# Kernel optimization log

Hardware: AMD Instinct MI355X
Metric: run time of the kernel (lower is better)

Reference implementation:

```python
import jax, jax.numpy as jnp
import numpy as np

N_NODES = 400      # total nodes across batch
B = 10             # graphs in batch (40 nodes each)
N_CONFIGS = 1000   # fixed by tile dataset
CONFIG_FEAT_DIM = 24
NODE_FEAT_DIM = 85  # continuous cols; node_feat has +1 col for shape-ele-type idx
N_SHAPE_TYPES = 8
SHAPE_EMB = 4
N_OPS = 120
OP_EMB = 32
H = 64             # h_dim
E = 800            # edges
CAT_DIM = NODE_FEAT_DIM + SHAPE_EMB + OP_EMB + CONFIG_FEAT_DIM  # 145


def _lin(k, i, o):
    return jax.random.normal(k, (i, o), jnp.float32) * (1.0 / np.sqrt(i))


def setup_inputs() -> dict:
    key = jax.random.key(0)
    ks = jax.random.split(key, 32)
    node_cont = jax.random.normal(ks[0], (N_NODES, NODE_FEAT_DIM), jnp.float32)
    shape_type = jax.random.randint(ks[1], (N_NODES, 1), 0, N_SHAPE_TYPES).astype(jnp.float32)
    node_feat = jnp.concatenate([node_cont, shape_type], axis=-1)  # [N, 86]
    node_opcode = jax.random.randint(ks[2], (N_NODES,), 0, N_OPS)
    config_feat = jax.random.normal(ks[3], (B * N_CONFIGS, CONFIG_FEAT_DIM), jnp.float32)
    edge_index = jax.random.randint(ks[4], (2, E), 0, N_NODES)
    batch = jnp.arange(N_NODES) // (N_NODES // B)  # 40 nodes per graph
    inp = dict(
        node_feat=node_feat, node_opcode=node_opcode, config_feat=config_feat,
        edge_index=edge_index, batch=batch,
        op_emb=jax.random.normal(ks[5], (N_OPS, OP_EMB), jnp.float32),
        shape_emb=jax.random.normal(ks[6], (N_SHAPE_TYPES, SHAPE_EMB), jnp.float32),
        W1=_lin(ks[7], CAT_DIM, 2 * H), b1=jnp.zeros((2 * H,), jnp.float32),
        W2=_lin(ks[8], 2 * H, 2 * H), b2=jnp.zeros((2 * H,), jnp.float32),
        Wl0=_lin(ks[9], 2 * H, H), Wr0=_lin(ks[10], 2 * H, H), bg0=jnp.zeros((H,), jnp.float32),
        Wl1=_lin(ks[11], H, H), Wr1=_lin(ks[12], H, H), bg1=jnp.zeros((H,), jnp.float32),
        Wl2=_lin(ks[13], H, H), Wr2=_lin(ks[14], H, H), bg2=jnp.zeros((H,), jnp.float32),
        Wp1=_lin(ks[15], H, H // 2), bp1=jnp.zeros((H // 2,), jnp.float32),
        Wp2=_lin(ks[16], H // 2, 1), bp2=jnp.zeros((1,), jnp.float32),
    )
    return inp


def _sage(x, src, dst, Wl, Wr, b, n):
    # PyG SAGEConv: lin_l(x) + lin_r(mean_{j->i} x_j), applied over [N, C, D]
    agg = jax.ops.segment_sum(x[src], dst, num_segments=n)
    deg = jax.ops.segment_sum(jnp.ones((src.shape[0],), x.dtype), dst, num_segments=n)
    mean = agg / jnp.maximum(deg, 1.0)[:, None, None]
    return x @ Wl + mean @ Wr + b


def reference(node_feat, node_opcode, config_feat, edge_index, batch,
              op_emb, shape_emb, W1, b1, W2, b2,
              Wl0, Wr0, bg0, Wl1, Wr1, bg1, Wl2, Wr2, bg2,
              Wp1, bp1, Wp2, bp2):
    n = node_feat.shape[0]
    cfg = config_feat.reshape(-1, N_CONFIGS, CONFIG_FEAT_DIM)  # [B, 1000, 24]
    ste = shape_emb[node_feat[:, -1].astype(jnp.int32)]        # [N, 4]
    op = op_emb[node_opcode]                                   # [N, 32]
    xn = jnp.concatenate([node_feat[:, :-1], ste, op], axis=-1)  # [N, 121]
    xn = jnp.broadcast_to(xn[:, None, :], (n, N_CONFIGS, xn.shape[-1]))
    xc = cfg[batch]  # repeat_interleave(cfg, n_nodes, dim=0) -> per-node config
    x = jnp.concatenate([xn, xc], axis=-1)                     # [N, 1000, 145]
    x = jax.nn.relu(x @ W1 + b1)
    x = jax.nn.relu(x @ W2 + b2)                               # [N, 1000, 128]
    src, dst = edge_index[0], edge_index[1]
    for Wl, Wr, bg in ((Wl0, Wr0, bg0), (Wl1, Wr1, bg1), (Wl2, Wr2, bg2)):
        x = jax.nn.relu(_sage(x, src, dst, Wl, Wr, bg, n))     # [N, 1000, 64]
    xf = x.reshape(n, -1)                                      # [N, 64000]
    cnt = jax.ops.segment_sum(jnp.ones((n,), xf.dtype), batch, num_segments=B)
    xg = jax.ops.segment_max(xf, batch, num_segments=B) \
         + jax.ops.segment_sum(xf, batch, num_segments=B) / jnp.maximum(cnt, 1.0)[:, None]
    xg = xg.reshape(B, N_CONFIGS, -1)                          # [B, 1000, 64]
    xg = xg / jnp.linalg.norm(xg, axis=-1, keepdims=True)
    out = (jax.nn.relu(xg @ Wp1 + bp1) @ Wp2 + bp2)[..., 0]    # [B, 1000]
    return out
```

## Files before the change

kernel.cpp:

```cpp
#include <hip/hip_runtime.h>
#include <hip/hip_bf16.h>

typedef unsigned short u16;
typedef short bf16x8 __attribute__((ext_vector_type(8)));
typedef float f32x4 __attribute__((ext_vector_type(4)));

#define NN 400
#define NB 10
#define NC 1000
#define CFD 24
#define NFD 85
#define NFROW 86
#define SEDIM 4
#define OEDIM 32
#define XND 121
#define EE 800
#define N_SHAPE_GUARD 7

__device__ __forceinline__ float b2f(u16 u) { return __uint_as_float((unsigned)u << 16); }
__device__ __forceinline__ u16 f2b(float v) {
  unsigned x = __float_as_uint(v);
  return (u16)((x + 0x7fff + ((x >> 16) & 1)) >> 16);
}
__device__ __forceinline__ float ldf(const void* p, int idx, int fz) {
  if (fz) return ((const float*)p)[idx];
  return b2f(((const u16*)p)[idx]);
}
__device__ __forceinline__ void stf(void* p, int idx, int fz, float v) {
  if (fz) { ((float*)p)[idx] = v; return; }
  ((u16*)p)[idx] = f2b(v);
}

__global__ void k_detect(const u16* __restrict__ w, int* __restrict__ flag) {
  int t = threadIdx.x;
  int wild = 0;
  for (int j = t; j < 512; j += 64) {
    float a = fabsf(b2f(w[j]));
    if (!(a < 1e4f)) wild++;
  }
  #pragma unroll
  for (int off = 32; off; off >>= 1) wild += __shfl_xor(wild, off);
  if (t == 0) *flag = (wild > 16) ? 1 : 0;
}

__global__ void k_prep(const void* __restrict__ node_feat, const int* __restrict__ opcode,
                       const void* __restrict__ op_emb, const void* __restrict__ shape_emb,
                       const void* __restrict__ W1, const void* __restrict__ b1,
                       const int* __restrict__ dflag, float* __restrict__ A_node) {
  __shared__ float xn[128];
  int fz = *dflag;
  int i = blockIdx.x, t = threadIdx.x;
  float v = 0.f;
  if (t < NFD) {
    v = ldf(node_feat, i*NFROW + t, fz);
  } else if (t < NFD + SEDIM) {
    int st = (int)ldf(node_feat, i*NFROW + NFD, fz);
    st = min(max(st, 0), N_SHAPE_GUARD);
    v = ldf(shape_emb, st*SEDIM + (t - NFD), fz);
  } else if (t < XND) {
    int oc = min(max(opcode[i], 0), 119);
    v = ldf(op_emb, oc*OEDIM + (t - NFD - SEDIM), fz);
  }
  xn[t] = v;
  __syncthreads();
  float acc = ldf(b1, t, fz);
  for (int k = 0; k < XND; k++) acc += xn[k] * ldf(W1, k*128 + t, fz);
  A_node[i*128 + t] = acc;
}

__global__ void k_cfg(const void* __restrict__ cfg, const void* __restrict__ W1,
                      const int* __restrict__ dflag, float* __restrict__ C_cfg) {
  int fz = *dflag;
  int r = blockIdx.x, t = threadIdx.x;
  __shared__ float cs[CFD];
  if (t < CFD) cs[t] = ldf(cfg, r*CFD + t, fz);
  __syncthreads();
  float acc = 0.f;
  for (int k = 0; k < CFD; k++) acc += cs[k] * ldf(W1, (XND + k)*128 + t, fz);
  C_cfg[r*128 + t] = acc;
}

__global__ void k_wpackT(const void* __restrict__ W2,
                         const void* __restrict__ Wl0, const void* __restrict__ Wr0,
                         const void* __restrict__ Wl1, const void* __restrict__ Wr1,
                         const void* __restrict__ Wl2, const void* __restrict__ Wr2,
                         const int* __restrict__ dflag,
                         u16* __restrict__ W2t, u16* __restrict__ Wc0t,
                         u16* __restrict__ Wc1t, u16* __restrict__ Wc2t) {
  int fz = *dflag;
  int idx = blockIdx.x * 256 + threadIdx.x;
  if (idx < 16384) {
    int n = idx >> 7, k = idx & 127;
    W2t[idx] = f2b(ldf(W2, k*128 + n, fz)); return;
  }
  idx -= 16384;
  if (idx < 16384) {
    int n = idx >> 7, k = idx & 127;
    float v = (n < 64) ? ldf(Wl0, k*64 + n, fz) : ldf(Wr0, k*64 + n - 64, fz);
    Wc0t[idx] = f2b(v); return;
  }
  idx -= 16384;
  if (idx < 8192) {
    int n = idx >> 6, k = idx & 63;
    float v = (n < 64) ? ldf(Wl1, k*64 + n, fz) : ldf(Wr1, k*64 + n - 64, fz);
    Wc1t[idx] = f2b(v); return;
  }
  idx -= 8192;
  if (idx < 8192) {
    int n = idx >> 6, k = idx & 63;
    float v = (n < 64) ? ldf(Wl2, k*64 + n, fz) : ldf(Wr2, k*64 + n - 64, fz);
    Wc2t[idx] = f2b(v); return;
  }
}

__global__ void k_csr(const int* __restrict__ edge_index, int* __restrict__ offs,
                      int* __restrict__ srcl) {
  __shared__ int cnt[NN];
  __shared__ int offl[NN + 1];
  int t = threadIdx.x;
  for (int i = t; i < NN; i += 256) cnt[i] = 0;
  __syncthreads();
  for (int e = t; e < EE; e += 256) {
    int d = edge_index[EE + e] & 511; if (d < NN) atomicAdd(&cnt[d], 1);
  }
  __syncthreads();
  if (t == 0) {
    int s = 0;
    for (int i = 0; i < NN; i++) { offl[i] = s; s += cnt[i]; }
    offl[NN] = s;
  }
  __syncthreads();
  for (int i = t; i < NN; i += 256) cnt[i] = offl[i];
  for (int i = t; i < NN + 1; i += 256) offs[i] = offl[i];
  __syncthreads();
  for (int e = t; e < EE; e += 256) {
    int d = edge_index[EE + e] & 511;
    if (d < NN) {
      int p = atomicAdd(&cnt[d], 1);
      srcl[p] = min(max(edge_index[e], 0), NN - 1);
    }
  }
}

__global__ __launch_bounds__(512, 1) void k_fused(
    const float* __restrict__ A_node, const float* __restrict__ C_cfg,
    const int* __restrict__ batch, const int* __restrict__ offs,
    const int* __restrict__ srcl,
    const u16* __restrict__ W2t, const u16* __restrict__ Wc0t,
    const u16* __restrict__ Wc1t, const u16* __restrict__ Wc2t,
    const void* __restrict__ b2, const void* __restrict__ bg0,
    const void* __restrict__ bg1, const void* __restrict__ bg2,
    const void* __restrict__ Wp1, const void* __restrict__ bp1,
    const void* __restrict__ Wp2, const void* __restrict__ bp2,
    const int* __restrict__ dflag, void* __restrict__ out) {
  __shared__ __align__(16) u16 xbuf[400 * 128];
  __shared__ __align__(16) u16 ybuf[400 * 64];
  __shared__ int offsl[401];
  __shared__ int srcll[EE];

  int c = blockIdx.x;
  int t = threadIdx.x;
  int w = t >> 6, l = t & 63;
  int lm = l & 15, quad = l >> 4;
  int fz = *dflag;

  float* cfgl = (float*)ybuf;
  for (int idx = t; idx < 1280; idx += 512)
    cfgl[idx] = C_cfg[((size_t)(idx >> 7) * NC + c) * 128 + (idx & 127)];
  for (int idx = t; idx < 401; idx += 512) offsl[idx] = offs[idx];
  for (int idx = t; idx < EE; idx += 512) srcll[idx] = srcl[idx];
  __syncthreads();

  {
    bf16x8 wf[8][4];
    #pragma unroll
    for (int mt = 0; mt < 8; mt++)
      #pragma unroll
      for (int kt = 0; kt < 4; kt++)
        wf[mt][kt] = *reinterpret_cast<const bf16x8*>(W2t + (mt*16 + lm)*128 + kt*32 + quad*8);
    float bv[8][4];
    #pragma unroll
    for (int mt = 0; mt < 8; mt++)
      #pragma unroll
      for (int rg = 0; rg < 4; rg++) bv[mt][rg] = ldf(b2, mt*16 + quad*4 + rg, fz);

    for (int tile = w; tile < 25; tile += 8) {
      int i = tile*16 + lm;
      int b = batch[i] % NB;
      const float* an = A_node + i*128;
      const float* cf = cfgl + b*128;
      bf16x8 bfr[4];
      #pragma unroll
      for (int kt = 0; kt < 4; kt++) {
        int ko = kt*32 + quad*8;
        float4 a0 = *(const float4*)(an + ko);
        float4 a1 = *(const float4*)(an + ko + 4);
        float4 c0 = *(const float4*)(cf + ko);
        float4 c1 = *(const float4*)(cf + ko + 4);
        bf16x8 f;
        f[0] = (short)f2b(fmaxf(a0.x + c0.x, 0.f));
        f[1] = (short)f2b(fmaxf(a0.y + c0.y, 0.f));
        f[2] = (short)f2b(fmaxf(a0.z + c0.z, 0.f));
        f[3] = (short)f2b(fmaxf(a0.w + c0.w, 0.f));
        f[4] = (short)f2b(fmaxf(a1.x + c1.x, 0.f));
        f[5] = (short)f2b(fmaxf(a1.y + c1.y, 0.f));
        f[6] = (short)f2b(fmaxf(a1.z + c1.z, 0.f));
        f[7] = (short)f2b(fmaxf(a1.w + c1.w, 0.f));
        bfr[kt] = f;
      }
      f32x4 acc[8] = {};
      #pragma unroll
      for (int kt = 0; kt < 4; kt++)
        #pragma unroll
        for (int mt = 0; mt < 8; mt++)
          acc[mt] = __builtin_amdgcn_mfma_f32_16x16x32_bf16(wf[mt][kt], bfr[kt], acc[mt], 0, 0, 0);
      #pragma unroll
      for (int mt = 0; mt < 8; mt++) {
        ushort4 s;
        s.x = f2b(fmaxf(acc[mt][0] + bv[mt][0], 0.f));
        s.y = f2b(fmaxf(acc[mt][1] + bv[mt][1], 0.f));
        s.z = f2b(fmaxf(acc[mt][2] + bv[mt][2], 0.f));
        s.w = f2b(fmaxf(acc[mt][3] + bv[mt][3], 0.f));
        int ch = mt*2 + (quad >> 1);
        int chs = ch ^ (i & 7);
        *reinterpret_cast<ushort4*>(&xbuf[i*128 + chs*8 + (quad & 1)*4]) = s;
      }
    }
  }
  __syncthreads();

  {
    bf16x8 wl[4][4], wr[4][4];
    #pragma unroll
    for (int mt = 0; mt < 4; mt++)
      #pragma unroll
      for (int kt = 0; kt < 4; kt++) {
        wl[mt][kt] = *reinterpret_cast<const bf16x8*>(Wc0t + (mt*16 + lm)*128 + kt*32 + quad*8);
        wr[mt][kt] = *reinterpret_cast<const bf16x8*>(Wc0t + (64 + mt*16 + lm)*128 + kt*32 + quad*8);
      }
    float bv[4][4];
    #pragma unroll
    for (int mt = 0; mt < 4; mt++)
      #pragma unroll
      for (int rg = 0; rg < 4; rg++) bv[mt][rg] = ldf(bg0, mt*16 + quad*4 + rg, fz);

    for (int tile = w; tile < 25; tile += 8) {
      int i = tile*16 + lm;
      int o0 = offsl[i], o1 = offsl[i + 1];
      float rd = 1.f / fmaxf((float)(o1 - o0), 1.f);
      bf16x8 xf[4], mf[4];
      #pragma unroll
      for (int kt = 0; kt < 4; kt++)
        xf[kt] = *reinterpret_cast<const bf16x8*>(&xbuf[i*128 + ((kt*4 + quad) ^ (i & 7))*8]);
      float s8[4][8] = {};
      int e = o0;
      for (; e + 1 < o1; e += 2) {
        int sn0 = srcll[e], sn1 = srcll[e + 1];
        bf16x8 z0[4], z1[4];
        #pragma unroll
        for (int kt = 0; kt < 4; kt++) {
          z0[kt] = *reinterpret_cast<const bf16x8*>(&xbuf[sn0*128 + ((kt*4 + quad) ^ (sn0 & 7))*8]);
          z1[kt] = *reinterpret_cast<const bf16x8*>(&xbuf[sn1*128 + ((kt*4 + quad) ^ (sn1 & 7))*8]);
        }
        #pragma unroll
        for (int kt = 0; kt < 4; kt++)
          #pragma unroll
          for (int j = 0; j < 8; j++) {
            s8[kt][j] += b2f((u16)z0[kt][j]);
            s8[kt][j] += b2f((u16)z1[kt][j]);
          }
      }
      if (e < o1) {
        int sn0 = srcll[e];
        #pragma unroll
        for (int kt = 0; kt < 4; kt++) {
          bf16x8 zv = *reinterpret_cast<const bf16x8*>(&xbuf[sn0*128 + ((kt*4 + quad) ^ (sn0 & 7))*8]);
          #pragma unroll
          for (int j = 0; j < 8; j++) s8[kt][j] += b2f((u16)zv[j]);
        }
      }
      #pragma unroll
      for (int kt = 0; kt < 4; kt++) {
        bf16x8 f;
        #pragma unroll
        for (int j = 0; j < 8; j++) f[j] = (short)f2b(s8[kt][j] * rd);
        mf[kt] = f;
      }
      f32x4 acc[4] = {};
      #pragma unroll
      for (int kt = 0; kt < 4; kt++)
        #pragma unroll
        for (int mt = 0; mt < 4; mt++) {
          acc[mt] = __builtin_amdgcn_mfma_f32_16x16x32_bf16(wl[mt][kt], xf[kt], acc[mt], 0, 0, 0);
          acc[mt] = __builtin_amdgcn_mfma_f32_16x16x32_bf16(wr[mt][kt], mf[kt], acc[mt], 0, 0, 0);
        }
      #pragma unroll
      for (int mt = 0; mt < 4; mt++) {
        ushort4 s;
        s.x = f2b(fmaxf(acc[mt][0] + bv[mt][0], 0.f));
        s.y = f2b(fmaxf(acc[mt][1] + bv[mt][1], 0.f));
        s.z = f2b(fmaxf(acc[mt][2] + bv[mt][2], 0.f));
        s.w = f2b(fmaxf(acc[mt][3] + bv[mt][3], 0.f));
        int ch = mt*2 + (quad >> 1);
        int chs = ch ^ (i & 7);
        *reinterpret_cast<ushort4*>(&ybuf[i*64 + chs*8 + (quad & 1)*4]) = s;
      }
    }
  }
  __syncthreads();

  u16* src_buf = ybuf;
  u16* dst_buf = xbuf;
  for (int layer = 0; layer < 2; layer++) {
    const u16* Wt = (layer == 0) ? Wc1t : Wc2t;
    const void* bg = (layer == 0) ? bg1 : bg2;
    bf16x8 wl[4][2], wr[4][2];
    #pragma unroll
    for (int mt = 0; mt < 4; mt++)
      #pragma unroll
      for (int kt = 0; kt < 2; kt++) {
        wl[mt][kt] = *reinterpret_cast<const bf16x8*>(Wt + (mt*16 + lm)*64 + kt*32 + quad*8);
        wr[mt][kt] = *reinterpret_cast<const bf16x8*>(Wt + (64 + mt*16 + lm)*64 + kt*32 + quad*8);
      }
    float bv[4][4];
    #pragma unroll
    for (int mt = 0; mt < 4; mt++)
      #pragma unroll
      for (int rg = 0; rg < 4; rg++) bv[mt][rg] = ldf(bg, mt*16 + quad*4 + rg, fz);

    for (int tile = w; tile < 25; tile += 8) {
      int i = tile*16 + lm;
      int o0 = offsl[i], o1 = offsl[i + 1];
      float rd = 1.f / fmaxf((float)(o1 - o0), 1.f);
      bf16x8 xf[2], mf[2];
      #pragma unroll
      for (int kt = 0; kt < 2; kt++)
        xf[kt] = *reinterpret_cast<const bf16x8*>(&src_buf[i*64 + ((kt*4 + quad) ^ (i & 7))*8]);
      float s8[2][8] = {};
      int e = o0;
      for (; e + 1 < o1; e += 2) {
        int sn0 = srcll[e], sn1 = srcll[e + 1];
        bf16x8 z0[2], z1[2];
        #pragma unroll
        for (int kt = 0; kt < 2; kt++) {
          z0[kt] = *reinterpret_cast<const bf16x8*>(&src_buf[sn0*64 + ((kt*4 + quad) ^ (sn0 & 7))*8]);
          z1[kt] = *reinterpret_cast<const bf16x8*>(&src_buf[sn1*64 + ((kt*4 + quad) ^ (sn1 & 7))*8]);
        }
        #pragma unroll
        for (int kt = 0; kt < 2; kt++)
          #pragma unroll
          for (int j = 0; j < 8; j++) {
            s8[kt][j] += b2f((u16)z0[kt][j]);
            s8[kt][j] += b2f((u16)z1[kt][j]);
          }
      }
      if (e < o1) {
        int sn0 = srcll[e];
        #pragma unroll
        for (int kt = 0; kt < 2; kt++) {
          bf16x8 zv = *reinterpret_cast<const bf16x8*>(&src_buf[sn0*64 + ((kt*4 + quad) ^ (sn0 & 7))*8]);
          #pragma unroll
          for (int j = 0; j < 8; j++) s8[kt][j] += b2f((u16)zv[j]);
        }
      }
      #pragma unroll
      for (int kt = 0; kt < 2; kt++) {
        bf16x8 f;
        #pragma unroll
        for (int j = 0; j < 8; j++) f[j] = (short)f2b(s8[kt][j] * rd);
        mf[kt] = f;
      }
      f32x4 acc[4] = {};
      #pragma unroll
      for (int kt = 0; kt < 2; kt++)
        #pragma unroll
        for (int mt = 0; mt < 4; mt++) {
          acc[mt] = __builtin_amdgcn_mfma_f32_16x16x32_bf16(wl[mt][kt], xf[kt], acc[mt], 0, 0, 0);
          acc[mt] = __builtin_amdgcn_mfma_f32_16x16x32_bf16(wr[mt][kt], mf[kt], acc[mt], 0, 0, 0);
        }
      #pragma unroll
      for (int mt = 0; mt < 4; mt++) {
        ushort4 s;
        s.x = f2b(fmaxf(acc[mt][0] + bv[mt][0], 0.f));
        s.y = f2b(fmaxf(acc[mt][1] + bv[mt][1], 0.f));
        s.z = f2b(fmaxf(acc[mt][2] + bv[mt][2], 0.f));
        s.w = f2b(fmaxf(acc[mt][3] + bv[mt][3], 0.f));
        int ch = mt*2 + (quad >> 1);
        int chs = ch ^ (i & 7);
        *reinterpret_cast<ushort4*>(&dst_buf[i*64 + chs*8 + (quad & 1)*4]) = s;
      }
    }
    __syncthreads();
    u16* tmp = src_buf; src_buf = dst_buf; dst_buf = tmp;
  }

  {
    float* scr  = (float*)xbuf;
    float* wp1s = (float*)&xbuf[4096];
    for (int idx = t; idx < 2048; idx += 512) wp1s[idx] = ldf(Wp1, idx, fz);
    __syncthreads();
    for (int b = w; b < NB; b += 8) {
      int h = l;
      float mx = -3.0e38f, sm = 0.f;
      for (int j = 0; j < 40; j++) {
        int row = b*40 + j;
        int chs = (h >> 3) ^ (row & 7);
        float v = b2f(src_buf[row*64 + chs*8 + (h & 7)]);
        mx = fmaxf(mx, v); sm += v;
      }
      float g = mx + sm * (1.f / 40.f);
      float sq = g * g;
      #pragma unroll
      for (int off = 32; off; off >>= 1) sq += __shfl_xor(sq, off);
      float gn = g * rsqrtf(sq);
      scr[w*64 + h] = gn;
      int j32 = l & 31;
      float hj = ldf(bp1, j32, fz);
      for (int k = 0; k < 64; k++) hj += scr[w*64 + k] * wp1s[k*32 + j32];
      hj = fmaxf(hj, 0.f);
      float contrib = hj * ldf(Wp2, j32, fz);
      #pragma unroll
      for (int off = 32; off; off >>= 1) contrib += __shfl_xor(contrib, off);
      if (l == 0) stf(out, b*NC + c, fz, contrib * 0.5f + ldf(bp2, 0, fz));
    }
  }
}

extern "C" void kernel_launch(void* const* d_in, const int* in_sizes, int n_in,
                              void* d_out, int out_size, void* d_ws, size_t ws_size,
                              hipStream_t stream) {
  const void* node_feat   = d_in[0];
  const int*  node_opcode = (const int*)d_in[1];
  const void* config_feat = d_in[2];
  const int*  edge_index  = (const int*)d_in[3];
  const int*  batch       = (const int*)d_in[4];
  const void* op_emb      = d_in[5];
  const void* shape_emb   = d_in[6];
  const void* W1  = d_in[7];
  const void* b1  = d_in[8];
  const void* W2  = d_in[9];
  const void* b2  = d_in[10];
  const void* Wl0 = d_in[11];
  const void* Wr0 = d_in[12];
  const void* bg0 = d_in[13];
  const void* Wl1 = d_in[14];
  const void* Wr1 = d_in[15];
  const void* bg1 = d_in[16];
  const void* Wl2 = d_in[17];
  const void* Wr2 = d_in[18];
  const void* bg2 = d_in[19];
  const void* Wp1 = d_in[20];
  const void* bp1 = d_in[21];
  const void* Wp2 = d_in[22];
  const void* bp2 = d_in[23];

  char* p = (char*)d_ws;
  int*   flag   = (int*)p;   p += 256;
  float* A_node = (float*)p; p += 400*128*4;
  float* C_cfg  = (float*)p; p += 10000*128*4;
  u16*   W2t    = (u16*)p;   p += 128*128*2;
  u16*   Wc0t   = (u16*)p;   p += 128*128*2;
  u16*   Wc1t   = (u16*)p;   p += 128*64*2;
  u16*   Wc2t   = (u16*)p;   p += 128*64*2;
  int*   offs   = (int*)p;   p += 2048;
  int*   srcl   = (int*)p;   p += 4096;

  k_detect<<<dim3(1), dim3(64), 0, stream>>>((const u16*)W1, flag);
  k_prep<<<dim3(400), dim3(128), 0, stream>>>(node_feat, node_opcode, op_emb, shape_emb, W1, b1, flag, A_node);
  k_cfg<<<dim3(10000), dim3(128), 0, stream>>>(config_feat, W1, flag, C_cfg);
  k_wpackT<<<dim3(192), dim3(256), 0, stream>>>(W2, Wl0, Wr0, Wl1, Wr1, Wl2, Wr2, flag, W2t, Wc0t, Wc1t, Wc2t);
  k_csr<<<dim3(1), dim3(256), 0, stream>>>(edge_index, offs, srcl);

  k_fused<<<dim3(1000), dim3(512), 0, stream>>>(
      A_node, C_cfg, batch, offs, srcl, W2t, Wc0t, Wc1t, Wc2t,
      b2, bg0, bg1, bg2, Wp1, bp1, Wp2, bp2, flag, d_out);
}
```

Measured before the change: 336.9 us.

## Merge prep kernels into one launch and double fused block to 1024 threads

New measurement: 782.2 us. 132% more time.

```diff
diff --git a/kernel.cpp b/kernel.cpp
--- a/kernel.cpp
+++ b/kernel.cpp
@@ -31,118 +31,126 @@
   ((u16*)p)[idx] = f2b(v);
 }
 
-__global__ void k_detect(const u16* __restrict__ w, int* __restrict__ flag) {
+__device__ __forceinline__ void detect_wave0(const void* W1, int t, int* flagl) {
+  if (t < 64) {
+    int wild = 0;
+    const u16* wv = (const u16*)W1;
+    for (int j = t; j < 512; j += 64) {
+      float a = fabsf(b2f(wv[j]));
+      if (!(a < 1e4f)) wild++;
+    }
+    #pragma unroll
+    for (int off = 32; off; off >>= 1) wild += __shfl_xor(wild, off);
+    if (t == 0) *flagl = (wild > 16) ? 1 : 0;
+  }
+}
+
+__global__ __launch_bounds__(256) void k_prep_all(
+    const void* __restrict__ node_feat, const int* __restrict__ opcode,
+    const void* __restrict__ cfg, const int* __restrict__ edge_index,
+    const void* __restrict__ op_emb, const void* __restrict__ shape_emb,
+    const void* __restrict__ W1, const void* __restrict__ b1,
+    const void* __restrict__ W2,
+    const void* __restrict__ Wl0, const void* __restrict__ Wr0,
+    const void* __restrict__ Wl1, const void* __restrict__ Wr1,
+    const void* __restrict__ Wl2, const void* __restrict__ Wr2,
+    float* __restrict__ A_node, float* __restrict__ C_cfg,
+    u16* __restrict__ W2t, u16* __restrict__ Wc0t,
+    u16* __restrict__ Wc1t, u16* __restrict__ Wc2t,
+    int* __restrict__ offs, int* __restrict__ srcl) {
+  __shared__ int flagl;
   int t = threadIdx.x;
-  int wild = 0;
-  for (int j = t; j < 512; j += 64) {
-    float a = fabsf(b2f(w[j]));
-    if (!(a < 1e4f)) wild++;
-  }
-  #pragma unroll
-  for (int off = 32; off; off >>= 1) wild += __shfl_xor(wild, off);
-  if (t == 0) *flag = (wild > 16) ? 1 : 0;
-}
-
-__global__ void k_prep(const void* __restrict__ node_feat, const int* __restrict__ opcode,
-                       const void* __restrict__ op_emb, const void* __restrict__ shape_emb,
-                       const void* __restrict__ W1, const void* __restrict__ b1,
-                       const int* __restrict__ dflag, float* __restrict__ A_node) {
-  __shared__ float xn[128];
-  int fz = *dflag;
-  int i = blockIdx.x, t = threadIdx.x;
-  float v = 0.f;
-  if (t < NFD) {
-    v = ldf(node_feat, i*NFROW + t, fz);
-  } else if (t < NFD + SEDIM) {
-    int st = (int)ldf(node_feat, i*NFROW + NFD, fz);
-    st = min(max(st, 0), N_SHAPE_GUARD);
-    v = ldf(shape_emb, st*SEDIM + (t - NFD), fz);
-  } else if (t < XND) {
-    int oc = min(max(opcode[i], 0), 119);
-    v = ldf(op_emb, oc*OEDIM + (t - NFD - SEDIM), fz);
-  }
-  xn[t] = v;
+  detect_wave0(W1, t, &flagl);
   __syncthreads();
-  float acc = ldf(b1, t, fz);
-  for (int k = 0; k < XND; k++) acc += xn[k] * ldf(W1, k*128 + t, fz);
-  A_node[i*128 + t] = acc;
-}
-
-__global__ void k_cfg(const void* __restrict__ cfg, const void* __restrict__ W1,
-                      const int* __restrict__ dflag, float* __restrict__ C_cfg) {
-  int fz = *dflag;
-  int r = blockIdx.x, t = threadIdx.x;
-  __shared__ float cs[CFD];
-  if (t < CFD) cs[t] = ldf(cfg, r*CFD + t, fz);
-  __syncthreads();
-  float acc = 0.f;
-  for (int k = 0; k < CFD; k++) acc += cs[k] * ldf(W1, (XND + k)*128 + t, fz);
-  C_cfg[r*128 + t] = acc;
-}
-
-__global__ void k_wpackT(const void* __restrict__ W2,
-                         const void* __restrict__ Wl0, const void* __restrict__ Wr0,
-                         const void* __restrict__ Wl1, const void* __restrict__ Wr1,
-                         const void* __restrict__ Wl2, const void* __restrict__ Wr2,
-                         const int* __restrict__ dflag,
-                         u16* __restrict__ W2t, u16* __restrict__ Wc0t,
-                         u16* __restrict__ Wc1t, u16* __restrict__ Wc2t) {
-  int fz = *dflag;
-  int idx = blockIdx.x * 256 + threadIdx.x;
-  if (idx < 16384) {
-    int n = idx >> 7, k = idx & 127;
-    W2t[idx] = f2b(ldf(W2, k*128 + n, fz)); return;
-  }
-  idx -= 16384;
-  if (idx < 16384) {
-    int n = idx >> 7, k = idx & 127;
-    float v = (n < 64) ? ldf(Wl0, k*64 + n, fz) : ldf(Wr0, k*64 + n - 64, fz);
-    Wc0t[idx] = f2b(v); return;
-  }
-  idx -= 16384;
-  if (idx < 8192) {
-    int n = idx >> 6, k = idx & 63;
-    float v = (n < 64) ? ldf(Wl1, k*64 + n, fz) : ldf(Wr1, k*64 + n - 64, fz);
-    Wc1t[idx] = f2b(v); return;
-  }
-  idx -= 8192;
-  if (idx < 8192) {
-    int n = idx >> 6, k = idx & 63;
-    float v = (n < 64) ? ldf(Wl2, k*64 + n, fz) : ldf(Wr2, k*64 + n - 64, fz);
-    Wc2t[idx] = f2b(v); return;
-  }
-}
-
-__global__ void k_csr(const int* __restrict__ edge_index, int* __restrict__ offs,
-                      int* __restrict__ srcl) {
-  __shared__ int cnt[NN];
-  __shared__ int offl[NN + 1];
-  int t = threadIdx.x;
-  for (int i = t; i < NN; i += 256) cnt[i] = 0;
-  __syncthreads();
-  for (int e = t; e < EE; e += 256) {
-    int d = edge_index[EE + e] & 511; if (d < NN) atomicAdd(&cnt[d], 1);
-  }
-  __syncthreads();
-  if (t == 0) {
-    int s = 0;
-    for (int i = 0; i < NN; i++) { offl[i] = s; s += cnt[i]; }
-    offl[NN] = s;
-  }
-  __syncthreads();
-  for (int i = t; i < NN; i += 256) cnt[i] = offl[i];
-  for (int i = t; i < NN + 1; i += 256) offs[i] = offl[i];
-  __syncthreads();
-  for (int e = t; e < EE; e += 256) {
-    int d = edge_index[EE + e] & 511;
-    if (d < NN) {
-      int p = atomicAdd(&cnt[d], 1);
-      srcl[p] = min(max(edge_index[e], 0), NN - 1);
-    }
-  }
-}
-
-__global__ __launch_bounds__(512, 1) void k_fused(
+  int fz = flagl;
+  int bid = blockIdx.x;
+
+  if (bid < 5000) {
+    int r = bid*2 + (t >> 7), col = t & 127;
+    float acc = 0.f;
+    #pragma unroll
+    for (int k = 0; k < CFD; k++)
+      acc += ldf(cfg, r*CFD + k, fz) * ldf(W1, (XND + k)*128 + col, fz);
+    C_cfg[r*128 + col] = acc;
+    return;
+  }
+  if (bid < 5200) {
+    __shared__ float xn[256];
+    int half = t >> 7, tt = t & 127;
+    int i = (bid - 5000)*2 + half;
+    float v = 0.f;
+    if (tt < NFD) {
+      v = ldf(node_feat, i*NFROW + tt, fz);
+    } else if (tt < NFD + SEDIM) {
+      int st = (int)ldf(node_feat, i*NFROW + NFD, fz);
+      st = min(max(st, 0), N_SHAPE_GUARD);
+      v = ldf(shape_emb, st*SEDIM + (tt - NFD), fz);
+    } else if (tt < XND) {
+      int oc = min(max(opcode[i], 0), 119);
+      v = ldf(op_emb, oc*OEDIM + (tt - NFD - SEDIM), fz);
+    }
+    xn[half*128 + tt] = v;
+    __syncthreads();
+    float acc = ldf(b1, tt, fz);
+    for (int k = 0; k < XND; k++) acc += xn[half*128 + k] * ldf(W1, k*128 + tt, fz);
+    A_node[i*128 + tt] = acc;
+    return;
+  }
+  if (bid < 5392) {
+    int idx = (bid - 5200)*256 + t;
+    if (idx < 16384) {
+      int n = idx >> 7, k = idx & 127;
+      W2t[idx] = f2b(ldf(W2, k*128 + n, fz)); return;
+    }
+    idx -= 16384;
+    if (idx < 16384) {
+      int n = idx >> 7, k = idx & 127;
+      float v = (n < 64) ? ldf(Wl0, k*64 + n, fz) : ldf(Wr0, k*64 + n - 64, fz);
+      Wc0t[idx] = f2b(v); return;
+    }
+    idx -= 16384;
+    if (idx < 8192) {
+      int n = idx >> 6, k = idx & 63;
+      float v = (n < 64) ? ldf(Wl1, k*64 + n, fz) : ldf(Wr1, k*64 + n - 64, fz);
+      Wc1t[idx] = f2b(v); return;
+    }
+    idx -= 8192;
+    if (idx < 8192) {
+      int n = idx >> 6, k = idx & 63;
+      float v = (n < 64) ? ldf(Wl2, k*64 + n, fz) : ldf(Wr2, k*64 + n - 64, fz);
+      Wc2t[idx] = f2b(v); return;
+    }
+    return;
+  }
+  {
+    __shared__ int cnt[NN];
+    __shared__ int offl[NN + 1];
+    for (int i = t; i < NN; i += 256) cnt[i] = 0;
+    __syncthreads();
+    for (int e = t; e < EE; e += 256) {
+      int d = edge_index[EE + e] & 511; if (d < NN) atomicAdd(&cnt[d], 1);
+    }
+    __syncthreads();
+    if (t == 0) {
+      int s = 0;
+      for (int i = 0; i < NN; i++) { offl[i] = s; s += cnt[i]; }
+      offl[NN] = s;
+    }
+    __syncthreads();
+    for (int i = t; i < NN; i += 256) cnt[i] = offl[i];
+    for (int i = t; i < NN + 1; i += 256) offs[i] = offl[i];
+    __syncthreads();
+    for (int e = t; e < EE; e += 256) {
+      int d = edge_index[EE + e] & 511;
+      if (d < NN) {
+        int p = atomicAdd(&cnt[d], 1);
+        srcl[p] = min(max(edge_index[e], 0), NN - 1);
+      }
+    }
+  }
+}
+
+__global__ __launch_bounds__(1024, 1) void k_fused(
     const float* __restrict__ A_node, const float* __restrict__ C_cfg,
     const int* __restrict__ batch, const int* __restrict__ offs,
     const int* __restrict__ srcl,
@@ -152,24 +160,26 @@
     const void* __restrict__ bg1, const void* __restrict__ bg2,
     const void* __restrict__ Wp1, const void* __restrict__ bp1,
     const void* __restrict__ Wp2, const void* __restrict__ bp2,
-    const int* __restrict__ dflag, void* __restrict__ out) {
+    const void* __restrict__ W1d, void* __restrict__ out) {
   __shared__ __align__(16) u16 xbuf[400 * 128];
   __shared__ __align__(16) u16 ybuf[400 * 64];
   __shared__ int offsl[401];
   __shared__ int srcll[EE];
+  __shared__ int flagl;
 
   int c = blockIdx.x;
   int t = threadIdx.x;
   int w = t >> 6, l = t & 63;
   int lm = l & 15, quad = l >> 4;
-  int fz = *dflag;
-
+
+  detect_wave0(W1d, t, &flagl);
   float* cfgl = (float*)ybuf;
-  for (int idx = t; idx < 1280; idx += 512)
+  for (int idx = t; idx < 1280; idx += 1024)
     cfgl[idx] = C_cfg[((size_t)(idx >> 7) * NC + c) * 128 + (idx & 127)];
-  for (int idx = t; idx < 401; idx += 512) offsl[idx] = offs[idx];
-  for (int idx = t; idx < EE; idx += 512) srcll[idx] = srcl[idx];
+  for (int idx = t; idx < 401; idx += 1024) offsl[idx] = offs[idx];
+  for (int idx = t; idx < EE; idx += 1024) srcll[idx] = srcl[idx];
   __syncthreads();
+  int fz = flagl;
 
   {
     bf16x8 wf[8][4];
@@ -184,7 +194,7 @@
       #pragma unroll
       for (int rg = 0; rg < 4; rg++) bv[mt][rg] = ldf(b2, mt*16 + quad*4 + rg, fz);
 
-    for (int tile = w; tile < 25; tile += 8) {
+    for (int tile = w; tile < 25; tile += 16) {
       int i = tile*16 + lm;
       int b = batch[i] % NB;
       const float* an = A_node + i*128;
@@ -244,7 +254,7 @@
       #pragma unroll
       for (int rg = 0; rg < 4; rg++) bv[mt][rg] = ldf(bg0, mt*16 + quad*4 + rg, fz);
 
-    for (int tile = w; tile < 25; tile += 8) {
+    for (int tile = w; tile < 25; tile += 16) {
       int i = tile*16 + lm;
       int o0 = offsl[i], o1 = offsl[i + 1];
       float rd = 1.f / fmaxf((float)(o1 - o0), 1.f);
@@ -328,7 +338,7 @@
       #pragma unroll
       for (int rg = 0; rg < 4; rg++) bv[mt][rg] = ldf(bg, mt*16 + quad*4 + rg, fz);
 
-    for (int tile = w; tile < 25; tile += 8) {
+    for (int tile = w; tile < 25; tile += 16) {
       int i = tile*16 + lm;
       int o0 = offsl[i], o1 = offsl[i + 1];
       float rd = 1.f / fmaxf((float)(o1 - o0), 1.f);
@@ -397,9 +407,9 @@
   {
     float* scr  = (float*)xbuf;
     float* wp1s = (float*)&xbuf[4096];
-    for (int idx = t; idx < 2048; idx += 512) wp1s[idx] = ldf(Wp1, idx, fz);
-    __syncthreads();
-    for (int b = w; b < NB; b += 8) {
+    for (int idx = t; idx < 2048; idx += 1024) wp1s[idx] = ldf(Wp1, idx, fz);
+    __syncthreads();
+    for (int b = w; b < NB; b += 16) {
       int h = l;
       float mx = -3.0e38f, sm = 0.f;
       for (int j = 0; j < 40; j++) {
@@ -455,7 +465,6 @@
   const void* bp2 = d_in[23];
 
   char* p = (char*)d_ws;
-  int*   flag   = (int*)p;   p += 256;
   float* A_node = (float*)p; p += 400*128*4;
   float* C_cfg  = (float*)p; p += 10000*128*4;
   u16*   W2t    = (u16*)p;   p += 128*128*2;
@@ -465,13 +474,12 @@
   int*   offs   = (int*)p;   p += 2048;
   int*   srcl   = (int*)p;   p += 4096;
 
-  k_detect<<<dim3(1), dim3(64), 0, stream>>>((const u16*)W1, flag);
-  k_prep<<<dim3(400), dim3(128), 0, stream>>>(node_feat, node_opcode, op_emb, shape_emb, W1, b1, flag, A_node);
-  k_cfg<<<dim3(10000), dim3(128), 0, stream>>>(config_feat, W1, flag, C_cfg);
-  k_wpackT<<<dim3(192), dim3(256), 0, stream>>>(W2, Wl0, Wr0, Wl1, Wr1, Wl2, Wr2, flag, W2t, Wc0t, Wc1t, Wc2t);
-  k_csr<<<dim3(1), dim3(256), 0, stream>>>(edge_index, offs, srcl);
-
-  k_fused<<<dim3(1000), dim3(512), 0, stream>>>(
+  k_prep_all<<<dim3(5393), dim3(256), 0, stream>>>(
+      node_feat, node_opcode, config_feat, edge_index, op_emb, shape_emb,
+      W1, b1, W2, Wl0, Wr0, Wl1, Wr1, Wl2, Wr2,
+      A_node, C_cfg, W2t, Wc0t, Wc1t, Wc2t, offs, srcl);
+
+  k_fused<<<dim3(1000), dim3(1024), 0, stream>>>(
       A_node, C_cfg, batch, offs, srcl, W2t, Wc0t, Wc1t, Wc2t,
-      b2, bg0, bg1, bg2, Wp1, bp1, Wp2, bp2, flag, d_out);
-}
+      b2, bg0, bg1, bg2, Wp1, bp1, Wp2, bp2, W1, d_out);
+}
```
